# Performance work log

Measured on AMD Instinct MI355X. Metric: run time of the kernel, lower is better.

## Reference

```python
import jax, jax.numpy as jnp
import numpy as np

N = 50000      # nodes
E = 640000     # edges
D = 128        # input_dim
O = 128        # output_dim
R = 8          # num_rels


def _uniform(k, shape, fan_in):
    s = 1.0 / np.sqrt(fan_in)
    return jax.random.uniform(k, shape, jnp.float32, -s, s)


def setup_inputs() -> dict:
    key = jax.random.key(0)
    ks = jax.random.split(key, 12)
    x = jax.random.normal(ks[0], (N, D), jnp.float32)
    src = jax.random.randint(ks[1], (E,), 0, N, jnp.int32)
    dst = jax.random.randint(ks[2], (E,), 0, N, jnp.int32)
    etype = jax.random.randint(ks[3], (E,), 0, R, jnp.int32)
    # TypedLinear relation weight bank [R, D, O]
    W_rel = _uniform(ks[4], (R, D, O), D)
    # w1: Linear(D, D)
    w1_W = _uniform(ks[5], (D, D), D)
    w1_b = _uniform(ks[6], (D,), D)
    # MLP (2 layers): Linear(D, O) -> relu -> Linear(O, O)
    m1_W = _uniform(ks[7], (D, O), D)
    m1_b = _uniform(ks[8], (O,), D)
    m2_W = _uniform(ks[9], (O, O), O)
    m2_b = _uniform(ks[10], (O,), O)
    return {"x": x, "src": src, "dst": dst, "etype": etype,
            "W_rel": W_rel, "w1_W": w1_W, "w1_b": w1_b,
            "m1_W": m1_W, "m1_b": m1_b, "m2_W": m2_W, "m2_b": m2_b}


def reference(x, src, dst, etype, W_rel, w1_W, w1_b, m1_W, m1_b, m2_W, m2_b):
    # TypedLinear message: m_e = x[src_e] @ W_rel[etype_e]
    # Since R is small, precompute all relation projections per node [N, R, O]
    # then gather per edge -- avoids materializing per-edge [E, D, O] weights.
    h_all = jnp.einsum('nd,rdo->nro', x, W_rel)          # [N, R, O]
    m = h_all[src, etype]                                 # [E, O] gather
    # scatter-sum aggregation into destination nodes
    agg = jax.ops.segment_sum(m, dst, num_segments=x.shape[0])  # [N, O]
    # update: w1(feat_in) + inneigh, then MLP (linear-relu-linear)
    h = x @ w1_W + w1_b + agg
    h = jax.nn.relu(h @ m1_W + m1_b)
    return h @ m2_W + m2_b
```

## Files before the change

### kernel.cpp

```cpp
#include <hip/hip_runtime.h>
#include <hip/hip_bf16.h>
#include <stdint.h>

#define N_NODES 50000
#define E_EDGES 640000
#define NB_TILES 782
#define NKEY 400000
#define NKEYP 400384
#define SCAN_BLOCKS 391

typedef __attribute__((ext_vector_type(8))) short short8;
typedef __attribute__((ext_vector_type(4))) float float4v;

__device__ __forceinline__ unsigned short f32_to_bf16(float f) {
  uint32_t u = __float_as_uint(f);
  u += 0x7fffu + ((u >> 16) & 1u);
  return (unsigned short)(u >> 16);
}

__global__ __launch_bounds__(256) void k0_tw(
    const float* __restrict__ W_rel, const float* __restrict__ w1W,
    const float* __restrict__ m1W, const float* __restrict__ m2W,
    unsigned short* __restrict__ wTg) {
  int m = blockIdx.x;
  const float* srcp = (m < 8) ? (W_rel + (size_t)m * 16384)
                              : (m == 8 ? w1W : (m == 9 ? m1W : m2W));
  unsigned short* dstp = wTg + (size_t)m * 16384;
  int tid = threadIdx.x;
  for (int i = 0; i < 64; ++i) {
    int idx = tid + i * 256;
    int o = idx >> 7, k = idx & 127;
    dstp[idx] = f32_to_bf16(srcp[k * 128 + o]);
  }
}

__global__ __launch_bounds__(256) void k_hist(
    const int* __restrict__ dst, const int* __restrict__ ety, int* __restrict__ cnt) {
  int e = blockIdx.x * 256 + threadIdx.x;
  if (e < E_EDGES) atomicAdd(&cnt[dst[e] * 8 + ety[e]], 1);
}

__global__ __launch_bounds__(1024) void k_scanA(
    const int* __restrict__ cnt, int* __restrict__ off, int* __restrict__ btot) {
  __shared__ int s[1024];
  int t = threadIdx.x, g = blockIdx.x * 1024 + t;
  int v = cnt[g];
  s[t] = v; __syncthreads();
  for (int d = 1; d < 1024; d <<= 1) {
    int a = (t >= d) ? s[t - d] : 0;
    __syncthreads();
    s[t] += a;
    __syncthreads();
  }
  off[g] = s[t] - v;
  if (t == 1023) btot[blockIdx.x] = s[t];
}

__global__ __launch_bounds__(512) void k_scanB(int* __restrict__ btot) {
  __shared__ int s[512];
  int t = threadIdx.x;
  int v = (t < SCAN_BLOCKS) ? btot[t] : 0;
  s[t] = v; __syncthreads();
  for (int d = 1; d < 512; d <<= 1) {
    int a = (t >= d) ? s[t - d] : 0;
    __syncthreads();
    s[t] += a;
    __syncthreads();
  }
  if (t < SCAN_BLOCKS) btot[t] = s[t] - v;
}

__global__ __launch_bounds__(1024) void k_scanC(
    int* __restrict__ off, const int* __restrict__ btot) {
  int g = blockIdx.x * 1024 + threadIdx.x;
  off[g] += btot[blockIdx.x];
}

__global__ __launch_bounds__(256) void k_fill(
    const int* __restrict__ src, const int* __restrict__ dst,
    const int* __restrict__ ety, const int* __restrict__ off,
    int* __restrict__ cur, int* __restrict__ eidx) {
  int e = blockIdx.x * 256 + threadIdx.x;
  if (e >= E_EDGES) return;
  int key = dst[e] * 8 + ety[e];
  int p = off[key] + atomicAdd(&cur[key], 1);
  eidx[p] = src[e] * 8 + ety[e];
}

__device__ __forceinline__ void load_x_tile(const float* __restrict__ x,
                                            short (*xs)[136], int tile0, int tid) {
  for (int i = 0; i < 16; ++i) {
    int idx = tid + i * 256;
    int row = idx >> 6, c2 = idx & 63;
    int node = tile0 + row;
    float2 v = make_float2(0.f, 0.f);
    if (node < N_NODES) v = *(const float2*)&x[(size_t)node * 128 + c2 * 2];
    uint32_t p = (uint32_t)f32_to_bf16(v.x) | ((uint32_t)f32_to_bf16(v.y) << 16);
    *(uint32_t*)&xs[row][c2 * 2] = p;
  }
}

__device__ __forceinline__ void load_w_tile(const unsigned short* __restrict__ wsrc,
                                            short (*wT)[136], int tid) {
  const uint32_t* s = (const uint32_t*)wsrc;
  #pragma unroll
  for (int i = 0; i < 32; ++i) {
    int idx = tid + i * 256;
    int n = idx >> 6, kw = idx & 63;
    *(uint32_t*)&wT[n][kw * 2] = s[idx];
  }
}

__device__ __forceinline__ void gemm_tile(const short (*A)[136], const short (*Bt)[136],
                                          int wave, int lane, float4v acc[8]) {
  int arow = wave * 16 + (lane & 15);
  int koff = (lane >> 4) * 8;
  #pragma unroll
  for (int kk = 0; kk < 4; ++kk) {
    short8 a = *(const short8*)&A[arow][kk * 32 + koff];
    #pragma unroll
    for (int n = 0; n < 8; ++n) {
      short8 b = *(const short8*)&Bt[n * 16 + (lane & 15)][kk * 32 + koff];
      acc[n] = __builtin_amdgcn_mfma_f32_16x16x32_bf16(a, b, acc[n], 0, 0, 0);
    }
  }
}

__global__ __launch_bounds__(256) void k1_hall(
    const float* __restrict__ x, const unsigned short* __restrict__ wTg,
    unsigned short* __restrict__ h_all) {
  __shared__ short xs[64][136];
  __shared__ short wT[128][136];
  __shared__ short hs[4][16][136];
  int tid = threadIdx.x, wave = tid >> 6, lane = tid & 63;
  int tile0 = blockIdx.x * 64;

  load_x_tile(x, xs, tile0, tid);

  for (int r = 0; r < 8; ++r) {
    __syncthreads();
    load_w_tile(wTg + (size_t)r * 16384, wT, tid);
    __syncthreads();

    float4v acc[8];
    #pragma unroll
    for (int n = 0; n < 8; ++n) acc[n] = (float4v){0.f, 0.f, 0.f, 0.f};
    gemm_tile(xs, wT, wave, lane, acc);

    #pragma unroll
    for (int n = 0; n < 8; ++n)
      #pragma unroll
      for (int i = 0; i < 4; ++i)
        hs[wave][(lane >> 4) * 4 + i][n * 16 + (lane & 15)] = (short)f32_to_bf16(acc[n][i]);
    #pragma unroll
    for (int i = 0; i < 16; ++i) {
      int node = tile0 + wave * 16 + i;
      if (node < N_NODES)
        ((uint32_t*)h_all)[((size_t)node * 8 + r) * 64 + lane] =
            *(const uint32_t*)&hs[wave][i][lane * 2];
    }
  }
}

__global__ __launch_bounds__(256) void k_agg(
    const unsigned short* __restrict__ h_all, const int* __restrict__ eidx,
    const int* __restrict__ off, float* __restrict__ agg) {
  int v = blockIdx.x * 4 + (threadIdx.x >> 6);
  if (v >= N_NODES) return;
  int lane = threadIdx.x & 63;
  int s0 = off[v * 8], s1 = off[v * 8 + 8];
  float a0 = 0.f, a1 = 0.f;
  for (int i = s0; i < s1; ++i) {
    uint32_t key = (uint32_t)eidx[i];
    uint32_t w = ((const uint32_t*)h_all)[(size_t)key * 64 + lane];
    a0 += __uint_as_float(w << 16);
    a1 += __uint_as_float(w & 0xffff0000u);
  }
  *(float2*)&agg[(size_t)v * 128 + lane * 2] = make_float2(a0, a1);
}

__global__ __launch_bounds__(256) void k3_update(
    const float* __restrict__ x, const float* __restrict__ agg,
    const unsigned short* __restrict__ wTg,
    const float* __restrict__ w1b, const float* __restrict__ m1b,
    const float* __restrict__ m2b, float* __restrict__ out) {
  __shared__ short xs[64][136];
  __shared__ short hs[64][136];
  __shared__ short wT[128][136];
  int tid = threadIdx.x, wave = tid >> 6, lane = tid & 63;
  int tile0 = blockIdx.x * 64;

  load_x_tile(x, xs, tile0, tid);
  load_w_tile(wTg + (size_t)8 * 16384, wT, tid);
  __syncthreads();

  float4v acc[8];

  #pragma unroll
  for (int n = 0; n < 8; ++n) acc[n] = (float4v){0.f, 0.f, 0.f, 0.f};
  gemm_tile(xs, wT, wave, lane, acc);
  #pragma unroll
  for (int n = 0; n < 8; ++n)
    #pragma unroll
    for (int i = 0; i < 4; ++i) {
      int row = wave * 16 + (lane >> 4) * 4 + i;
      int col = n * 16 + (lane & 15);
      int node = tile0 + row;
      float a = (node < N_NODES) ? agg[(size_t)node * 128 + col] : 0.f;
      hs[row][col] = (short)f32_to_bf16(acc[n][i] + w1b[col] + a);
    }
  __syncthreads();

  load_w_tile(wTg + (size_t)9 * 16384, wT, tid);
  __syncthreads();
  #pragma unroll
  for (int n = 0; n < 8; ++n) acc[n] = (float4v){0.f, 0.f, 0.f, 0.f};
  gemm_tile(hs, wT, wave, lane, acc);
  #pragma unroll
  for (int n = 0; n < 8; ++n)
    #pragma unroll
    for (int i = 0; i < 4; ++i) {
      int row = wave * 16 + (lane >> 4) * 4 + i;
      int col = n * 16 + (lane & 15);
      float v = acc[n][i] + m1b[col];
      xs[row][col] = (short)f32_to_bf16(v > 0.f ? v : 0.f);
    }
  __syncthreads();

  load_w_tile(wTg + (size_t)10 * 16384, wT, tid);
  __syncthreads();
  #pragma unroll
  for (int n = 0; n < 8; ++n) acc[n] = (float4v){0.f, 0.f, 0.f, 0.f};
  gemm_tile(xs, wT, wave, lane, acc);
  #pragma unroll
  for (int n = 0; n < 8; ++n)
    #pragma unroll
    for (int i = 0; i < 4; ++i) {
      int row = wave * 16 + (lane >> 4) * 4 + i;
      int col = n * 16 + (lane & 15);
      int node = tile0 + row;
      if (node < N_NODES) out[(size_t)node * 128 + col] = acc[n][i] + m2b[col];
    }
}

extern "C" void kernel_launch(void* const* d_in, const int* in_sizes, int n_in,
                              void* d_out, int out_size, void* d_ws, size_t ws_size,
                              hipStream_t stream) {
  const float* x     = (const float*)d_in[0];
  const int*   src   = (const int*)d_in[1];
  const int*   dst   = (const int*)d_in[2];
  const int*   ety   = (const int*)d_in[3];
  const float* W_rel = (const float*)d_in[4];
  const float* w1b   = (const float*)d_in[6];
  const float* m1b   = (const float*)d_in[8];
  const float* m2b   = (const float*)d_in[10];
  const float* w1W   = (const float*)d_in[5];
  const float* m1W   = (const float*)d_in[7];
  const float* m2W   = (const float*)d_in[9];
  float* out = (float*)d_out;

  char* ws = (char*)d_ws;
  unsigned short* wTg   = (unsigned short*)ws;
  unsigned short* h_all = (unsigned short*)(ws + 524288);
  float*          agg   = (float*)(ws + 102924288);
  int*            cnt   = (int*)(ws + 128524288);
  int*            off   = (int*)(ws + 130125824);
  int*            btot  = (int*)(ws + 131727360);
  int*            cur   = (int*)(ws + 131731456);
  int*            eidx  = (int*)(ws + 133331456);

  hipMemsetAsync(cnt, 0, (size_t)NKEYP * 4, stream);
  hipMemsetAsync(cur, 0, (size_t)NKEY * 4, stream);

  k0_tw<<<11, 256, 0, stream>>>(W_rel, w1W, m1W, m2W, wTg);
  k_hist<<<E_EDGES / 256, 256, 0, stream>>>(dst, ety, cnt);
  k_scanA<<<SCAN_BLOCKS, 1024, 0, stream>>>(cnt, off, btot);
  k_scanB<<<1, 512, 0, stream>>>(btot);
  k_scanC<<<SCAN_BLOCKS, 1024, 0, stream>>>(off, btot);
  k_fill<<<E_EDGES / 256, 256, 0, stream>>>(src, dst, ety, off, cur, eidx);
  k1_hall<<<NB_TILES, 256, 0, stream>>>(x, wTg, h_all);
  k_agg<<<(N_NODES + 3) / 4, 256, 0, stream>>>(h_all, eidx, off, agg);
  k3_update<<<NB_TILES, 256, 0, stream>>>(x, agg, wTg, w1b, m1b, m2b, out);
}
```

Before: 342.8 us.

## Aggregate raw features per relation before projection and fuse into update kernel

Swaps the order of projection and aggregation: for each relation it sums bf16 source-node features per destination, then multiplies by that relation's weight. It also folds the x@w1 term into the same accumulator and fuses everything into the MLP kernel. This drops the large per-node, per-relation h_all buffer and the separate aggregation buffer, and shrinks the gathered rows from projected outputs to raw features. The fill kernel now advances the offsets atomically in place of the separate cursor array, and x is converted to bf16 once up front. The cost is that aggregation sums are rounded to bf16 before the GEMM, and the per-tile gather loop is serial within each wave.

Result: slower. 539.2 us (+57.3%).

```diff
diff --git a/kernel.cpp b/kernel.cpp
--- a/kernel.cpp
+++ b/kernel.cpp
@@ -16,6 +16,15 @@
   uint32_t u = __float_as_uint(f);
   u += 0x7fffu + ((u >> 16) & 1u);
   return (unsigned short)(u >> 16);
+}
+
+__global__ __launch_bounds__(256) void kx_cvt(
+    const float* __restrict__ x, unsigned short* __restrict__ xb) {
+  int idx = blockIdx.x * 256 + threadIdx.x;
+  float4 v = ((const float4*)x)[idx];
+  uint32_t p0 = (uint32_t)f32_to_bf16(v.x) | ((uint32_t)f32_to_bf16(v.y) << 16);
+  uint32_t p1 = (uint32_t)f32_to_bf16(v.z) | ((uint32_t)f32_to_bf16(v.w) << 16);
+  ((uint2*)xb)[idx] = make_uint2(p0, p1);
 }
 
 __global__ __launch_bounds__(256) void k0_tw(
@@ -78,26 +87,13 @@
 
 __global__ __launch_bounds__(256) void k_fill(
     const int* __restrict__ src, const int* __restrict__ dst,
-    const int* __restrict__ ety, const int* __restrict__ off,
-    int* __restrict__ cur, int* __restrict__ eidx) {
+    const int* __restrict__ ety, int* __restrict__ off,
+    int* __restrict__ eidx) {
   int e = blockIdx.x * 256 + threadIdx.x;
   if (e >= E_EDGES) return;
   int key = dst[e] * 8 + ety[e];
-  int p = off[key] + atomicAdd(&cur[key], 1);
-  eidx[p] = src[e] * 8 + ety[e];
-}
-
-__device__ __forceinline__ void load_x_tile(const float* __restrict__ x,
-                                            short (*xs)[136], int tile0, int tid) {
-  for (int i = 0; i < 16; ++i) {
-    int idx = tid + i * 256;
-    int row = idx >> 6, c2 = idx & 63;
-    int node = tile0 + row;
-    float2 v = make_float2(0.f, 0.f);
-    if (node < N_NODES) v = *(const float2*)&x[(size_t)node * 128 + c2 * 2];
-    uint32_t p = (uint32_t)f32_to_bf16(v.x) | ((uint32_t)f32_to_bf16(v.y) << 16);
-    *(uint32_t*)&xs[row][c2 * 2] = p;
-  }
+  int p = atomicAdd(&off[key], 1);
+  eidx[p] = src[e];
 }
 
 __device__ __forceinline__ void load_w_tile(const unsigned short* __restrict__ wsrc,
@@ -126,78 +122,60 @@
   }
 }
 
-__global__ __launch_bounds__(256) void k1_hall(
-    const float* __restrict__ x, const unsigned short* __restrict__ wTg,
-    unsigned short* __restrict__ h_all) {
-  __shared__ short xs[64][136];
-  __shared__ short wT[128][136];
-  __shared__ short hs[4][16][136];
-  int tid = threadIdx.x, wave = tid >> 6, lane = tid & 63;
-  int tile0 = blockIdx.x * 64;
-
-  load_x_tile(x, xs, tile0, tid);
-
-  for (int r = 0; r < 8; ++r) {
-    __syncthreads();
-    load_w_tile(wTg + (size_t)r * 16384, wT, tid);
-    __syncthreads();
-
-    float4v acc[8];
-    #pragma unroll
-    for (int n = 0; n < 8; ++n) acc[n] = (float4v){0.f, 0.f, 0.f, 0.f};
-    gemm_tile(xs, wT, wave, lane, acc);
-
-    #pragma unroll
-    for (int n = 0; n < 8; ++n)
-      #pragma unroll
-      for (int i = 0; i < 4; ++i)
-        hs[wave][(lane >> 4) * 4 + i][n * 16 + (lane & 15)] = (short)f32_to_bf16(acc[n][i]);
-    #pragma unroll
-    for (int i = 0; i < 16; ++i) {
-      int node = tile0 + wave * 16 + i;
-      if (node < N_NODES)
-        ((uint32_t*)h_all)[((size_t)node * 8 + r) * 64 + lane] =
-            *(const uint32_t*)&hs[wave][i][lane * 2];
-    }
-  }
-}
-
-__global__ __launch_bounds__(256) void k_agg(
-    const unsigned short* __restrict__ h_all, const int* __restrict__ eidx,
-    const int* __restrict__ off, float* __restrict__ agg) {
-  int v = blockIdx.x * 4 + (threadIdx.x >> 6);
-  if (v >= N_NODES) return;
-  int lane = threadIdx.x & 63;
-  int s0 = off[v * 8], s1 = off[v * 8 + 8];
-  float a0 = 0.f, a1 = 0.f;
-  for (int i = s0; i < s1; ++i) {
-    uint32_t key = (uint32_t)eidx[i];
-    uint32_t w = ((const uint32_t*)h_all)[(size_t)key * 64 + lane];
-    a0 += __uint_as_float(w << 16);
-    a1 += __uint_as_float(w & 0xffff0000u);
-  }
-  *(float2*)&agg[(size_t)v * 128 + lane * 2] = make_float2(a0, a1);
-}
-
-__global__ __launch_bounds__(256) void k3_update(
-    const float* __restrict__ x, const float* __restrict__ agg,
-    const unsigned short* __restrict__ wTg,
+__global__ __launch_bounds__(256, 3) void k_fused(
+    const unsigned short* __restrict__ xb, const unsigned short* __restrict__ wTg,
+    const int* __restrict__ off, const int* __restrict__ cnt,
+    const int* __restrict__ eidx,
     const float* __restrict__ w1b, const float* __restrict__ m1b,
     const float* __restrict__ m2b, float* __restrict__ out) {
   __shared__ short xs[64][136];
-  __shared__ short hs[64][136];
   __shared__ short wT[128][136];
   int tid = threadIdx.x, wave = tid >> 6, lane = tid & 63;
   int tile0 = blockIdx.x * 64;
 
-  load_x_tile(x, xs, tile0, tid);
+  float4v acc[8];
+  #pragma unroll
+  for (int n = 0; n < 8; ++n) acc[n] = (float4v){0.f, 0.f, 0.f, 0.f};
+
+  for (int r = 0; r < 8; ++r) {
+    int e1[16], c[16];
+    #pragma unroll
+    for (int i = 0; i < 16; ++i) {
+      int node = tile0 + wave * 16 + i;
+      if (node < N_NODES) {
+        int key = node * 8 + r;
+        e1[i] = off[key]; c[i] = cnt[key];
+      } else { e1[i] = 0; c[i] = 0; }
+    }
+    load_w_tile(wTg + (size_t)r * 16384, wT, tid);
+
+    #pragma unroll 1
+    for (int i = 0; i < 16; ++i) {
+      int row = wave * 16 + i;
+      float a0 = 0.f, a1 = 0.f;
+      for (int j = e1[i] - c[i]; j < e1[i]; ++j) {
+        int s = eidx[j];
+        uint32_t w = ((const uint32_t*)xb)[(size_t)s * 64 + lane];
+        a0 += __uint_as_float(w << 16);
+        a1 += __uint_as_float(w & 0xffff0000u);
+      }
+      uint32_t p = (uint32_t)f32_to_bf16(a0) | ((uint32_t)f32_to_bf16(a1) << 16);
+      *(uint32_t*)&xs[row][lane * 2] = p;
+    }
+    __syncthreads();
+    gemm_tile(xs, wT, wave, lane, acc);
+    __syncthreads();
+  }
+
   load_w_tile(wTg + (size_t)8 * 16384, wT, tid);
-  __syncthreads();
-
-  float4v acc[8];
-
-  #pragma unroll
-  for (int n = 0; n < 8; ++n) acc[n] = (float4v){0.f, 0.f, 0.f, 0.f};
+  for (int i = 0; i < 16; ++i) {
+    int idx = tid + i * 256;
+    int row = idx >> 6, cc = idx & 63;
+    int node = tile0 + row;
+    uint32_t p = (node < N_NODES) ? ((const uint32_t*)xb)[(size_t)node * 64 + cc] : 0u;
+    *(uint32_t*)&xs[row][cc * 2] = p;
+  }
+  __syncthreads();
   gemm_tile(xs, wT, wave, lane, acc);
   #pragma unroll
   for (int n = 0; n < 8; ++n)
@@ -205,9 +183,7 @@
     for (int i = 0; i < 4; ++i) {
       int row = wave * 16 + (lane >> 4) * 4 + i;
       int col = n * 16 + (lane & 15);
-      int node = tile0 + row;
-      float a = (node < N_NODES) ? agg[(size_t)node * 128 + col] : 0.f;
-      hs[row][col] = (short)f32_to_bf16(acc[n][i] + w1b[col] + a);
+      xs[row][col] = (short)f32_to_bf16(acc[n][i] + w1b[col]);
     }
   __syncthreads();
 
@@ -215,7 +191,7 @@
   __syncthreads();
   #pragma unroll
   for (int n = 0; n < 8; ++n) acc[n] = (float4v){0.f, 0.f, 0.f, 0.f};
-  gemm_tile(hs, wT, wave, lane, acc);
+  gemm_tile(xs, wT, wave, lane, acc);
   #pragma unroll
   for (int n = 0; n < 8; ++n)
     #pragma unroll
@@ -251,34 +227,30 @@
   const int*   dst   = (const int*)d_in[2];
   const int*   ety   = (const int*)d_in[3];
   const float* W_rel = (const float*)d_in[4];
+  const float* w1W   = (const float*)d_in[5];
   const float* w1b   = (const float*)d_in[6];
+  const float* m1W   = (const float*)d_in[7];
   const float* m1b   = (const float*)d_in[8];
+  const float* m2W   = (const float*)d_in[9];
   const float* m2b   = (const float*)d_in[10];
-  const float* w1W   = (const float*)d_in[5];
-  const float* m1W   = (const float*)d_in[7];
-  const float* m2W   = (const float*)d_in[9];
   float* out = (float*)d_out;
 
   char* ws = (char*)d_ws;
-  unsigned short* wTg   = (unsigned short*)ws;
-  unsigned short* h_all = (unsigned short*)(ws + 524288);
-  float*          agg   = (float*)(ws + 102924288);
-  int*            cnt   = (int*)(ws + 128524288);
-  int*            off   = (int*)(ws + 130125824);
-  int*            btot  = (int*)(ws + 131727360);
-  int*            cur   = (int*)(ws + 131731456);
-  int*            eidx  = (int*)(ws + 133331456);
+  unsigned short* wTg  = (unsigned short*)ws;
+  unsigned short* xb   = (unsigned short*)(ws + 524288);
+  int*            cnt  = (int*)(ws + 13324288);
+  int*            off  = (int*)(ws + 14925824);
+  int*            btot = (int*)(ws + 16527360);
+  int*            eidx = (int*)(ws + 16531456);
 
   hipMemsetAsync(cnt, 0, (size_t)NKEYP * 4, stream);
-  hipMemsetAsync(cur, 0, (size_t)NKEY * 4, stream);
-
+  kx_cvt<<<6250, 256, 0, stream>>>(x, xb);
   k0_tw<<<11, 256, 0, stream>>>(W_rel, w1W, m1W, m2W, wTg);
   k_hist<<<E_EDGES / 256, 256, 0, stream>>>(dst, ety, cnt);
   k_scanA<<<SCAN_BLOCKS, 1024, 0, stream>>>(cnt, off, btot);
   k_scanB<<<1, 512, 0, stream>>>(btot);
   k_scanC<<<SCAN_BLOCKS, 1024, 0, stream>>>(off, btot);
-  k_fill<<<E_EDGES / 256, 256, 0, stream>>>(src, dst, ety, off, cur, eidx);
-  k1_hall<<<NB_TILES, 256, 0, stream>>>(x, wTg, h_all);
-  k_agg<<<(N_NODES + 3) / 4, 256, 0, stream>>>(h_all, eidx, off, agg);
-  k3_update<<<NB_TILES, 256, 0, stream>>>(x, agg, wTg, w1b, m1b, m2b, out);
-}
+  k_fill<<<E_EDGES / 256, 256, 0, stream>>>(src, dst, ety, off, eidx);
+  k_fused<<<NB_TILES, 256, 0, stream>>>(xb, wTg, off, cnt, eidx,
+                                        w1b, m1b, m2b, out);
+}
```
